# Optimization experiments

Measured on AMD Instinct MI355X. Metric: run time of the kernel, lower is better.

Reference implementation:

```python
import jax, jax.numpy as jnp
import numpy as np

B, S, E, H, FF = 4, 2048, 1024, 16, 4096
TD = 32  # transition_dim


def _layer_norm(v, g, b, eps=1e-5):
    m = v.mean(-1, keepdims=True)
    var = ((v - m) ** 2).mean(-1, keepdims=True)
    return (v - m) * jax.lax.rsqrt(var + eps) * g + b


def setup_inputs() -> dict:
    key = jax.random.key(0)
    ks = jax.random.split(key, 8)
    w = 0.02
    return {
        "x": jax.random.normal(ks[0], (B, S, E), dtype=jnp.float32),
        "transition_dim": TD,
        "ln1_g": jnp.ones((E,), jnp.float32),
        "ln1_b": jnp.zeros((E,), jnp.float32),
        "ln2_g": jnp.ones((E,), jnp.float32),
        "ln2_b": jnp.zeros((E,), jnp.float32),
        "w_qkv": jax.random.normal(ks[1], (3 * E, E), jnp.float32) * w,
        "b_qkv": jnp.zeros((3 * E,), jnp.float32),
        "w_o": jax.random.normal(ks[2], (E, E), jnp.float32) * w,
        "b_o": jnp.zeros((E,), jnp.float32),
        "w_fc1": jax.random.normal(ks[3], (FF, E), jnp.float32) * w,
        "b_fc1": jnp.zeros((FF,), jnp.float32),
        "w_fc2": jax.random.normal(ks[4], (E, FF), jnp.float32) * w,
        "b_fc2": jnp.zeros((E,), jnp.float32),
    }


def reference(x, transition_dim, ln1_g, ln1_b, ln2_g, ln2_b, w_qkv, b_qkv,
              w_o, b_o, w_fc1, b_fc1, w_fc2, b_fc2):
    Bx, Sx, Ex = x.shape
    Dh = Ex // H
    xn = _layer_norm(x, ln1_g, ln1_b)
    qkv = xn @ w_qkv.T + b_qkv                      # [B,S,3E]
    q, k, v = jnp.split(qkv, 3, axis=-1)
    def heads(t):
        return t.reshape(Bx, Sx, H, Dh).transpose(0, 2, 1, 3)  # [B,H,S,Dh]
    q, k, v = heads(q), heads(k), heads(v)
    scores = jnp.einsum("bhqd,bhkd->bhqk", q, k) / np.sqrt(Dh).astype(np.float32)
    # custom mask: causal (j > i) OR periodic value-column (j % TD == TD-1) blocked
    i = jnp.arange(Sx)
    mask = (i[None, :] > i[:, None]) | ((i[None, :] % transition_dim) == transition_dim - 1)
    scores = jnp.where(mask[None, None], -jnp.inf, scores)
    p = jax.nn.softmax(scores, axis=-1)
    attn = jnp.einsum("bhqk,bhkd->bhqd", p, v)
    attn = attn.transpose(0, 2, 1, 3).reshape(Bx, Sx, Ex)
    attn = attn @ w_o.T + b_o
    x = x + attn
    h = _layer_norm(x, ln2_g, ln2_b)
    h = jax.nn.gelu(h @ w_fc1.T + b_fc1, approximate=False) @ w_fc2.T + b_fc2
    return x + h
```

## Files before the change

### kernel.cpp

```cpp
#include <hip/hip_runtime.h>
#include <hip/hip_bf16.h>

typedef unsigned short u16;
typedef unsigned int u32;
typedef short bf16x8 __attribute__((ext_vector_type(8)));
typedef float f32x4 __attribute__((ext_vector_type(4)));
typedef float f32x16 __attribute__((ext_vector_type(16)));

#define B_ 4
#define S_ 2048
#define E_ 1024
#define H_ 16
#define FF_ 4096
#define M_ 8192

__device__ __forceinline__ u16 f2bf(float f) {
    u32 u = __float_as_uint(f);
    u32 r = (u + 0x7FFFu + ((u >> 16) & 1u)) >> 16;
    return (u16)r;
}
__device__ __forceinline__ float bf2f(u16 v) {
    return __uint_as_float(((u32)v) << 16);
}
__device__ __forceinline__ u32 cvtpk(float lo, float hi) {
    u32 r;
    asm("v_cvt_pk_bf16_f32 %0, %1, %2" : "=v"(r) : "v"(lo), "v"(hi));
    return r;
}
__device__ __forceinline__ void pswap(u32& a, u32& b) {
    asm("v_permlane32_swap_b32 %0, %1" : "+v"(a), "+v"(b));
}
__device__ __forceinline__ void gload16(const void* g, void* l) {
    __builtin_amdgcn_global_load_lds(
        (__attribute__((address_space(1))) void*)g,
        (__attribute__((address_space(3))) void*)l, 16, 0, 0);
}

__global__ __launch_bounds__(256) void cvt_kernel(const float* __restrict__ in,
                                                  u16* __restrict__ out, int n4) {
    int i = blockIdx.x * 256 + threadIdx.x;
    if (i < n4) {
        float4 v = ((const float4*)in)[i];
        ushort4 o;
        o.x = f2bf(v.x); o.y = f2bf(v.y); o.z = f2bf(v.z); o.w = f2bf(v.w);
        ((ushort4*)out)[i] = o;
    }
}

__global__ __launch_bounds__(256) void ln_kernel(const float* __restrict__ x,
                                                 const float* __restrict__ g,
                                                 const float* __restrict__ bb,
                                                 u16* __restrict__ out) {
    int row = blockIdx.x;
    int t = threadIdx.x;
    const float4* xr = (const float4*)(x + (size_t)row * E_);
    float4 v = xr[t];
    float s = v.x + v.y + v.z + v.w;
    float sq = v.x * v.x + v.y * v.y + v.z * v.z + v.w * v.w;
    for (int o = 1; o < 64; o <<= 1) {
        s += __shfl_xor(s, o, 64);
        sq += __shfl_xor(sq, o, 64);
    }
    __shared__ float ss[4], sqs[4];
    int w = t >> 6, l = t & 63;
    if (l == 0) { ss[w] = s; sqs[w] = sq; }
    __syncthreads();
    s = ss[0] + ss[1] + ss[2] + ss[3];
    sq = sqs[0] + sqs[1] + sqs[2] + sqs[3];
    float mean = s * (1.0f / E_);
    float var = sq * (1.0f / E_) - mean * mean;
    float rstd = rsqrtf(var + 1e-5f);
    float4 gv = ((const float4*)g)[t];
    float4 bv = ((const float4*)bb)[t];
    ushort4 o4;
    o4.x = f2bf((v.x - mean) * rstd * gv.x + bv.x);
    o4.y = f2bf((v.y - mean) * rstd * gv.y + bv.y);
    o4.z = f2bf((v.z - mean) * rstd * gv.z + bv.z);
    o4.w = f2bf((v.w - mean) * rstd * gv.w + bv.w);
    ((ushort4*)(out + (size_t)row * E_))[t] = o4;
}

template <int EPI, int BN>
__global__ __launch_bounds__(512, 2) void gemm256(const u16* __restrict__ A,
                                                  const u16* __restrict__ Bt,
                                                  const float* __restrict__ bias,
                                                  void* __restrict__ outp,
                                                  const float* __restrict__ resid,
                                                  u16* __restrict__ vt,
                                                  int N, int K) {
    constexpr int NF = BN / 64;
    __shared__ u16 ldsA[2 * 2 * 8192];
    __shared__ u16 ldsB[BN == 256 ? 2 * 2 * 8192 : 2 * 8192];
    int t = threadIdx.x;
    int wid = t >> 6, l = t & 63, l15 = l & 15, hi4 = l >> 4;
    int wm = wid >> 2, wn = wid & 3;

    int nwg = gridDim.x;
    int flat = blockIdx.x;
    int swz = (flat & 7) * (nwg >> 3) + (flat >> 3);
    int nx = N / BN;
    int m0 = (swz / nx) * 256, n0 = (swz % nx) * BN;
    const size_t Kb = (size_t)K * 2;

    f32x4 acc[8][NF];
    f32x4 zf = {0.f, 0.f, 0.f, 0.f};
#pragma unroll
    for (int i = 0; i < 8; i++)
#pragma unroll
        for (int j = 0; j < NF; j++) acc[i][j] = zf;

    auto stageA = [&](int buf, int h, int k0) {
#pragma unroll
        for (int rr = 0; rr < 2; ++rr) {
            int o = t * 16 + rr * 8192;
            int lr = o >> 7;
            int gch = ((o >> 4) & 7) ^ (lr & 7);
            int grow = m0 + (lr >> 6) * 128 + h * 64 + (lr & 63);
            gload16((const char*)A + (size_t)grow * Kb + k0 * 2 + gch * 16,
                    (char*)ldsA + (buf * 2 + h) * 16384 + o);
        }
    };
    auto stageB256 = [&](int buf, int h, int k0) {
#pragma unroll
        for (int rr = 0; rr < 2; ++rr) {
            int o = t * 16 + rr * 8192;
            int lr = o >> 7;
            int gch = ((o >> 4) & 7) ^ (lr & 7);
            int grow = n0 + (lr >> 5) * 64 + h * 32 + (lr & 31);
            gload16((const char*)Bt + (size_t)grow * Kb + k0 * 2 + gch * 16,
                    (char*)ldsB + (buf * 2 + h) * 16384 + o);
        }
    };
    auto stageB128 = [&](int buf, int k0) {
#pragma unroll
        for (int rr = 0; rr < 2; ++rr) {
            int o = t * 16 + rr * 8192;
            int lr = o >> 7;
            int gch = ((o >> 4) & 7) ^ (lr & 7);
            int grow = n0 + lr;
            gload16((const char*)Bt + (size_t)grow * Kb + k0 * 2 + gch * 16,
                    (char*)ldsB + buf * 16384 + o);
        }
    };

    auto readA = [&](int bq, int mh, bf16x8 (&af)[4][2]) {
#pragma unroll
        for (int mi = 0; mi < 4; mi++)
#pragma unroll
            for (int ks = 0; ks < 2; ks++) {
                int lr = wm * 64 + mi * 16 + l15;
                int ob = lr * 128 + ks * 64 + hi4 * 16;
                af[mi][ks] = *(const bf16x8*)((const char*)ldsA +
                             (bq * 2 + mh) * 16384 + (ob ^ ((lr & 7) << 4)));
            }
    };
    auto readB256 = [&](int bq, int nh, bf16x8 (&bfr)[2][2]) {
#pragma unroll
        for (int nq = 0; nq < 2; nq++)
#pragma unroll
            for (int ks = 0; ks < 2; ks++) {
                int lr = wn * 32 + nq * 16 + l15;
                int ob = lr * 128 + ks * 64 + hi4 * 16;
                bfr[nq][ks] = *(const bf16x8*)((const char*)ldsB +
                              (bq * 2 + nh) * 16384 + (ob ^ ((lr & 7) << 4)));
            }
    };
    auto readB128 = [&](int bq, bf16x8 (&bfr)[2][2]) {
#pragma unroll
        for (int nq = 0; nq < 2; nq++)
#pragma unroll
            for (int ks = 0; ks < 2; ks++) {
                int lr = wn * 32 + nq * 16 + l15;
                int ob = lr * 128 + ks * 64 + hi4 * 16;
                bfr[nq][ks] = *(const bf16x8*)((const char*)ldsB +
                              bq * 16384 + (ob ^ ((lr & 7) << 4)));
            }
    };
    auto mma = [&](bf16x8 (&af)[4][2], bf16x8 (&bfr)[2][2], int mh, int nh) {
#pragma unroll
        for (int mi = 0; mi < 4; mi++)
#pragma unroll
            for (int nq = 0; nq < 2; nq++)
#pragma unroll
                for (int ks = 0; ks < 2; ks++)
                    acc[mh * 4 + mi][nh * 2 + nq] =
                        __builtin_amdgcn_mfma_f32_16x16x32_bf16(
                            af[mi][ks], bfr[nq][ks], acc[mh * 4 + mi][nh * 2 + nq], 0, 0, 0);
    };

#define GWAIT(N)                                            \
    asm volatile("s_waitcnt vmcnt(" #N ")" ::: "memory");   \
    __builtin_amdgcn_sched_barrier(0);
#define PH_MID                                              \
    __builtin_amdgcn_s_barrier();                           \
    asm volatile("s_waitcnt lgkmcnt(0)" ::: "memory");      \
    __builtin_amdgcn_sched_barrier(0);                      \
    __builtin_amdgcn_s_setprio(1);
#define PH_END                                              \
    __builtin_amdgcn_s_setprio(0);                          \
    __builtin_amdgcn_s_barrier();

    int KT = K >> 6, ITERS = KT >> 1;

    if constexpr (BN == 256) {
        stageB256(0, 0, 0); stageB256(0, 1, 0); stageA(0, 0, 0); stageA(0, 1, 0);
        stageB256(1, 0, 64); stageB256(1, 1, 64); stageA(1, 0, 64);
        GWAIT(6);
        __builtin_amdgcn_s_barrier();
        for (int s = 0; s < ITERS; ++s) {
            int k1 = (2 * s + 1) << 6;
            int k2 = (2 * s + 2) << 6; if (k2 >= K) k2 = 0;
            int k3 = (2 * s + 3) << 6; if (k3 >= K) k3 = 0;
            bf16x8 af[4][2], b0[2][2], b1[2][2];
            readA(0, 0, af); readB256(0, 0, b0); stageA(1, 1, k1);
            PH_MID; mma(af, b0, 0, 0); PH_END;
            readB256(0, 1, b1); stageB256(0, 0, k2);
            PH_MID; mma(af, b1, 0, 1); PH_END;
            readA(0, 1, af); stageB256(0, 1, k2);
            PH_MID; mma(af, b0, 1, 0); PH_END;
            stageA(0, 0, k2); GWAIT(6);
            PH_MID; mma(af, b1, 1, 1); PH_END;
            readA(1, 0, af); readB256(1, 0, b0); stageA(0, 1, k2);
            PH_MID; mma(af, b0, 0, 0); PH_END;
            readB256(1, 1, b1); stageB256(1, 0, k3);
            PH_MID; mma(af, b1, 0, 1); PH_END;
            readA(1, 1, af); stageB256(1, 1, k3);
            PH_MID; mma(af, b0, 1, 0); PH_END;
            stageA(1, 0, k3); GWAIT(6);
            PH_MID; mma(af, b1, 1, 1); PH_END;
        }
    } else {
        stageB128(0, 0); stageA(0, 0, 0); stageA(0, 1, 0);
        stageB128(1, 64); stageA(1, 0, 64);
        GWAIT(4);
        __builtin_amdgcn_s_barrier();
        for (int s = 0; s < ITERS; ++s) {
            int k1 = (2 * s + 1) << 6;
            int k2 = (2 * s + 2) << 6; if (k2 >= K) k2 = 0;
            int k3 = (2 * s + 3) << 6; if (k3 >= K) k3 = 0;
            bf16x8 af[4][2], br[2][2];
            readA(0, 0, af); readB128(0, br); stageA(1, 1, k1);
            PH_MID; mma(af, br, 0, 0); PH_END;
            readA(0, 1, af); stageB128(0, k2); stageA(0, 0, k2); GWAIT(4);
            PH_MID; mma(af, br, 1, 0); PH_END;
            readA(1, 0, af); readB128(1, br); stageA(0, 1, k2);
            PH_MID; mma(af, br, 0, 0); PH_END;
            readA(1, 1, af); stageB128(1, k3); stageA(1, 0, k3); GWAIT(4);
            PH_MID; mma(af, br, 1, 0); PH_END;
        }
    }
#undef GWAIT
#undef PH_MID
#undef PH_END

    float bias_v[NF];
#pragma unroll
    for (int nf = 0; nf < NF; nf++) bias_v[nf] = bias[n0 + wn * (NF * 16) + nf * 16 + l15];

    if constexpr (EPI == 3) {
#pragma unroll
        for (int mf = 0; mf < 8; mf++)
#pragma unroll
            for (int nf = 0; nf < NF; nf++) {
                int col = n0 + wn * (NF * 16) + nf * 16 + l15;
                int row0 = m0 + wm * 128 + mf * 16 + hi4 * 4;
                ushort4 sv;
                u16* o16 = (u16*)outp;
#pragma unroll
                for (int j = 0; j < 4; j++) {
                    float v = acc[mf][nf][j] + bias_v[nf];
                    u16 r = f2bf(v);
                    o16[(size_t)(row0 + j) * N + col] = r;
                    ((u16*)&sv)[j] = r;
                }
                if (col >= 2048) {
                    int bb = row0 >> 11, s0r = row0 & 2047;
                    *(ushort4*)&vt[(((size_t)(bb << 10) + (col - 2048)) << 11) + s0r] = sv;
                }
            }
    } else {
#pragma unroll
        for (int mf = 0; mf < 8; mf++)
#pragma unroll
            for (int nf = 0; nf < NF; nf++)
#pragma unroll
                for (int j = 0; j < 4; j++) {
                    int row = m0 + wm * 128 + mf * 16 + hi4 * 4 + j;
                    int col = n0 + wn * (NF * 16) + nf * 16 + l15;
                    float v = acc[mf][nf][j] + bias_v[nf];
                    size_t idx = (size_t)row * N + col;
                    if (EPI == 2) v = 0.5f * v * (1.0f + erff(v * 0.70710678118f));
                    if (EPI == 1)
                        ((float*)outp)[idx] = resid[idx] + v;
                    else
                        ((u16*)outp)[idx] = f2bf(v);
                }
    }
}

__global__ __launch_bounds__(128) void attn_kernel(const u16* __restrict__ qkv,
                                                   const u16* __restrict__ vt,
                                                   u16* __restrict__ aout) {
    __shared__ u16 Ksb[2 * 4096];
    __shared__ u16 Vsb[2 * 4096];
    int t = threadIdx.x;
    int wv = t >> 6, l = t & 63;
    int q31 = l & 31, hi = l >> 5;
    int flat = blockIdx.x;
    int logical = (flat & 7) * 256 + (flat >> 3);
    int bh = logical >> 5;
    int qt = 31 - (logical & 31);
    int b = bh >> 4, h = bh & 15;
    int rowq = qt * 64 + wv * 32 + q31;

    const float qs = 0.18033688011f;
    const float THR = 44.3616f;

    bf16x8 qreg[4];
    const u16* qbase = qkv + (size_t)(b * S_ + rowq) * 3072 + h * 64 + hi * 8;
#pragma unroll
    for (int g = 0; g < 4; g++) qreg[g] = *(const bf16x8*)(qbase + 16 * g);

    const char* srcK0 = (const char*)(qkv + E_ + (size_t)(b * S_ + (t >> 3)) * 3072 + h * 64) +
                        ((t & 7) ^ ((t >> 3) & 7)) * 16;
    const char* srcV0 = (const char*)(vt + ((size_t)(bh * 64 + (t >> 3))) * 2048) +
                        ((t & 7) ^ ((t >> 3) & 7)) * 16;
    auto issueK = [&](int buf, int j0) {
#pragma unroll
        for (int pp = 0; pp < 4; pp++)
            gload16(srcK0 + (size_t)pp * 98304 + (size_t)j0 * 6144,
                    (char*)Ksb + buf * 8192 + 16 * t + 2048 * pp);
    };
    auto issueV = [&](int buf, int j0) {
#pragma unroll
        for (int pp = 0; pp < 4; pp++)
            gload16(srcV0 + (size_t)pp * 65536 + (size_t)j0 * 2,
                    (char*)Vsb + buf * 8192 + 16 * t + 2048 * pp);
    };

    f32x16 zf16;
#pragma unroll
    for (int r = 0; r < 16; r++) zf16[r] = 0.f;
    f32x16 o0 = zf16, o1 = zf16;
    float mrun = -INFINITY, lrun = 0.f;

    int j1 = (qt >= 1) ? 64 : 0;
    issueK(0, 0); issueV(0, 0);
    issueK(1, j1); issueV(1, j1);

    for (int jt = 0; jt <= qt; ++jt) {
        int cur = jt & 1;
        int j0 = jt * 64;
        asm volatile("s_waitcnt vmcnt(8)" ::: "memory");
        __builtin_amdgcn_sched_barrier(0);
        __builtin_amdgcn_s_barrier();

        const u16* Kc = Ksb + cur * 4096;
        const u16* Vc = Vsb + cur * 4096;

        f32x16 s0 = zf16, s1 = zf16;
        __builtin_amdgcn_s_setprio(1);
#pragma unroll
        for (int g = 0; g < 4; g++) {
            int r0 = q31, r1 = 32 + q31;
            bf16x8 k0 = *(const bf16x8*)&Kc[((r0 << 6) + hi * 8 + 16 * g) ^ ((r0 & 7) << 3)];
            bf16x8 k1 = *(const bf16x8*)&Kc[((r1 << 6) + hi * 8 + 16 * g) ^ ((r1 & 7) << 3)];
            s0 = __builtin_amdgcn_mfma_f32_32x32x16_bf16(k0, qreg[g], s0, 0, 0, 0);
            s1 = __builtin_amdgcn_mfma_f32_32x32x16_bf16(k1, qreg[g], s1, 0, 0, 0);
        }
        __builtin_amdgcn_s_setprio(0);

        float mx = -INFINITY;
        int cb0 = j0 + 4 * hi;
        if (jt == qt) {
#pragma unroll
            for (int r = 0; r < 16; r++) {
                const int cc = (r & 3) + 8 * (r >> 2);
                float v0 = s0[r], v1 = s1[r];
                bool bad0 = (cb0 + cc > rowq) || (r == 15 && hi);
                bool bad1 = (cb0 + 32 + cc > rowq) || (r == 15 && hi);
                v0 = bad0 ? -INFINITY : v0;
                v1 = bad1 ? -INFINITY : v1;
                s0[r] = v0; s1[r] = v1;
                mx = fmaxf(mx, fmaxf(v0, v1));
            }
        } else {
#pragma unroll
            for (int r = 0; r < 16; r++) {
                float v0 = s0[r], v1 = s1[r];
                if (r == 15) {
                    v0 = hi ? -INFINITY : v0;
                    v1 = hi ? -INFINITY : v1;
                    s0[r] = v0; s1[r] = v1;
                }
                mx = fmaxf(mx, fmaxf(v0, v1));
            }
        }
        mx = fmaxf(mx, __shfl_xor(mx, 32, 64));

        bool dokeep = __all(mx <= mrun + THR);
        if (!dokeep) {
            float mnew = fmaxf(mrun, mx);
            float sc = __builtin_amdgcn_exp2f((mrun - mnew) * qs);
#pragma unroll
            for (int r = 0; r < 16; r++) { o0[r] *= sc; o1[r] *= sc; }
            lrun *= sc;
            mrun = mnew;
        }
        float mq = mrun * qs;

        float sa = 0.f, sb = 0.f, sc2 = 0.f, sd = 0.f;
#pragma unroll
        for (int r = 0; r < 16; r++) {
            float p0 = __builtin_amdgcn_exp2f(fmaf(s0[r], qs, -mq));
            float p1 = __builtin_amdgcn_exp2f(fmaf(s1[r], qs, -mq));
            s0[r] = p0; s1[r] = p1;
            if (r & 1) { sb += p0; sd += p1; } else { sa += p0; sc2 += p1; }
        }
        lrun += (sa + sb) + (sc2 + sd);

        bf16x8 pa[4];
#pragma unroll
        for (int g = 0; g < 4; g++) {
            const int bs = (g & 1) * 8;
            u32 wa, wb, wc, wd;
            if (g < 2) {
                wa = cvtpk(s0[bs + 0], s0[bs + 1]);
                wb = cvtpk(s0[bs + 4], s0[bs + 5]);
                wc = cvtpk(s0[bs + 2], s0[bs + 3]);
                wd = cvtpk(s0[bs + 6], s0[bs + 7]);
            } else {
                wa = cvtpk(s1[bs + 0], s1[bs + 1]);
                wb = cvtpk(s1[bs + 4], s1[bs + 5]);
                wc = cvtpk(s1[bs + 2], s1[bs + 3]);
                wd = cvtpk(s1[bs + 6], s1[bs + 7]);
            }
            pswap(wa, wb);
            pswap(wc, wd);
            union { u32 w[4]; bf16x8 f; } u;
            u.w[0] = wa; u.w[1] = wc; u.w[2] = wb; u.w[3] = wd;
            pa[g] = u.f;
        }

        __builtin_amdgcn_s_setprio(1);
#pragma unroll
        for (int g = 0; g < 4; g++) {
            int d0 = q31, d1 = 32 + q31;
            bf16x8 v0 = *(const bf16x8*)&Vc[((d0 << 6) + hi * 8 + 16 * g) ^ ((d0 & 7) << 3)];
            bf16x8 v1 = *(const bf16x8*)&Vc[((d1 << 6) + hi * 8 + 16 * g) ^ ((d1 & 7) << 3)];
            o0 = __builtin_amdgcn_mfma_f32_32x32x16_bf16(v0, pa[g], o0, 0, 0, 0);
            o1 = __builtin_amdgcn_mfma_f32_32x32x16_bf16(v1, pa[g], o1, 0, 0, 0);
        }
        __builtin_amdgcn_s_setprio(0);

        __builtin_amdgcn_s_barrier();
        int nj = (jt + 2 <= qt) ? (jt + 2) * 64 : 0;
        issueK(cur, nj);
        issueV(cur, nj);
    }

    lrun += __shfl_xor(lrun, 32, 64);
    float inv = 1.0f / lrun;
    u16* orow = aout + (size_t)(b * S_ + rowq) * E_ + h * 64 + 4 * hi;
#pragma unroll
    for (int r = 0; r < 16; r++) {
        const int cc = (r & 3) + 8 * (r >> 2);
        orow[cc] = f2bf(o0[r] * inv);
        orow[32 + cc] = f2bf(o1[r] * inv);
    }
}

extern "C" void kernel_launch(void* const* d_in, const int* in_sizes, int n_in,
                              void* d_out, int out_size, void* d_ws, size_t ws_size,
                              hipStream_t stream) {
    const float* x = (const float*)d_in[0];
    const float* ln1_g = (const float*)d_in[2];
    const float* ln1_b = (const float*)d_in[3];
    const float* ln2_g = (const float*)d_in[4];
    const float* ln2_b = (const float*)d_in[5];
    const float* w_qkv = (const float*)d_in[6];
    const float* b_qkv = (const float*)d_in[7];
    const float* w_o = (const float*)d_in[8];
    const float* b_o = (const float*)d_in[9];
    const float* w_fc1 = (const float*)d_in[10];
    const float* b_fc1 = (const float*)d_in[11];
    const float* w_fc2 = (const float*)d_in[12];
    const float* b_fc2 = (const float*)d_in[13];
    float* out = (float*)d_out;
    char* ws = (char*)d_ws;

    u16* wqkv_bf = (u16*)(ws);
    u16* wo_bf   = (u16*)(ws + 6291456);
    u16* wfc1_bf = (u16*)(ws + 8388608);
    u16* wfc2_bf = (u16*)(ws + 16777216);
    u16* xn_bf   = (u16*)(ws + 25165824);
    u16* qkv_bf  = (u16*)(ws + 41943040);
    u16* ffn1_bf = (u16*)(ws + 41943040);
    u16* attn_bf = (u16*)(ws + 92274688);
    float* x2    = (float*)(ws + 109051904);
    u16* vtw     = (u16*)(ws + 109051904);
    (void)in_sizes; (void)n_in; (void)out_size; (void)ws_size;

    cvt_kernel<<<3072, 256, 0, stream>>>(w_qkv, wqkv_bf, 786432);
    cvt_kernel<<<1024, 256, 0, stream>>>(w_o, wo_bf, 262144);
    cvt_kernel<<<4096, 256, 0, stream>>>(w_fc1, wfc1_bf, 1048576);
    cvt_kernel<<<4096, 256, 0, stream>>>(w_fc2, wfc2_bf, 1048576);

    ln_kernel<<<M_, 256, 0, stream>>>(x, ln1_g, ln1_b, xn_bf);

    gemm256<3, 256><<<384, 512, 0, stream>>>(xn_bf, wqkv_bf, b_qkv, qkv_bf, nullptr, vtw, 3072, 1024);

    attn_kernel<<<2048, 128, 0, stream>>>(qkv_bf, vtw, attn_bf);

    gemm256<1, 128><<<256, 512, 0, stream>>>(attn_bf, wo_bf, b_o, x2, x, nullptr, 1024, 1024);

    ln_kernel<<<M_, 256, 0, stream>>>(x2, ln2_g, ln2_b, xn_bf);

    gemm256<2, 256><<<512, 512, 0, stream>>>(xn_bf, wfc1_bf, b_fc1, ffn1_bf, nullptr, nullptr, 4096, 1024);

    gemm256<1, 128><<<256, 512, 0, stream>>>(ffn1_bf, wfc2_bf, b_fc2, out, x2, nullptr, 1024, 4096);
}
```

Before: 407.5 us.

## Pair causal query tiles per attention block, split V transpose, merge weight casts

The attention kernel now has each block handle two query tiles, p0 and 31-p0, one after the other, so every block does the same amount of causal work, and the grid is halved to 1024 blocks. The V transpose moves out of the QKV GEMM epilogue, which did scattered ushort4 stores, into its own LDS-tiled transpose kernel. The four weight cast launches are merged into one. The cost is an extra kernel launch and a second read of the V slice, in exchange for better load balance and a simpler GEMM epilogue.

```diff
diff --git a/kernel.cpp b/kernel.cpp
--- a/kernel.cpp
+++ b/kernel.cpp
@@ -36,15 +36,49 @@
         (__attribute__((address_space(3))) void*)l, 16, 0, 0);
 }
 
-__global__ __launch_bounds__(256) void cvt_kernel(const float* __restrict__ in,
-                                                  u16* __restrict__ out, int n4) {
-    int i = blockIdx.x * 256 + threadIdx.x;
-    if (i < n4) {
-        float4 v = ((const float4*)in)[i];
-        ushort4 o;
-        o.x = f2bf(v.x); o.y = f2bf(v.y); o.z = f2bf(v.z); o.w = f2bf(v.w);
-        ((ushort4*)out)[i] = o;
+__global__ __launch_bounds__(256) void cvt4_kernel(const float* __restrict__ s0, u16* __restrict__ d0,
+                                                   const float* __restrict__ s1, u16* __restrict__ d1,
+                                                   const float* __restrict__ s2, u16* __restrict__ d2,
+                                                   const float* __restrict__ s3, u16* __restrict__ d3) {
+    int blk = blockIdx.x;
+    const float* s; u16* d; int base;
+    if (blk < 3072)      { s = s0; d = d0; base = blk; }
+    else if (blk < 4096) { s = s1; d = d1; base = blk - 3072; }
+    else if (blk < 8192) { s = s2; d = d2; base = blk - 4096; }
+    else                 { s = s3; d = d3; base = blk - 8192; }
+    int i = base * 256 + threadIdx.x;
+    float4 v = ((const float4*)s)[i];
+    ushort4 o;
+    o.x = f2bf(v.x); o.y = f2bf(v.y); o.z = f2bf(v.z); o.w = f2bf(v.w);
+    ((ushort4*)d)[i] = o;
+}
+
+__global__ __launch_bounds__(256) void vtrans_kernel(const u16* __restrict__ qkv,
+                                                     u16* __restrict__ vt) {
+    __shared__ u16 tile[64 * 67];
+    int t = threadIdx.x;
+    int st = blockIdx.x;
+    int bh = blockIdx.y;
+    int b = bh >> 4, h = bh & 15;
+    int s0 = st * 64;
+    int r = t >> 3, c0 = (t & 7) * 8;
+#pragma unroll
+    for (int half = 0; half < 2; half++) {
+        int rr = r + half * 32;
+        const u16* src = qkv + (size_t)(b * S_ + s0 + rr) * 3072 + 2048 + h * 64 + c0;
+        uint4 v = *(const uint4*)src;
+        u16* pv = (u16*)&v;
+#pragma unroll
+        for (int e = 0; e < 8; e++) tile[(c0 + e) * 67 + rr] = pv[e];
     }
+    __syncthreads();
+    int d = t >> 2, ch = t & 3;
+    u16 buf[16];
+#pragma unroll
+    for (int j = 0; j < 16; j++) buf[j] = tile[d * 67 + ch * 16 + j];
+    u16* dst = vt + ((size_t)bh * 64 + d) * 2048 + s0 + ch * 16;
+    *(uint4*)dst = *(uint4*)&buf[0];
+    *(uint4*)(dst + 8) = *(uint4*)&buf[8];
 }
 
 __global__ __launch_bounds__(256) void ln_kernel(const float* __restrict__ x,
@@ -86,7 +120,6 @@
                                                   const float* __restrict__ bias,
                                                   void* __restrict__ outp,
                                                   const float* __restrict__ resid,
-                                                  u16* __restrict__ vt,
                                                   int N, int K) {
     constexpr int NF = BN / 64;
     __shared__ u16 ldsA[2 * 2 * 8192];
@@ -257,45 +290,22 @@
 #pragma unroll
     for (int nf = 0; nf < NF; nf++) bias_v[nf] = bias[n0 + wn * (NF * 16) + nf * 16 + l15];
 
-    if constexpr (EPI == 3) {
-#pragma unroll
-        for (int mf = 0; mf < 8; mf++)
-#pragma unroll
-            for (int nf = 0; nf < NF; nf++) {
+#pragma unroll
+    for (int mf = 0; mf < 8; mf++)
+#pragma unroll
+        for (int nf = 0; nf < NF; nf++)
+#pragma unroll
+            for (int j = 0; j < 4; j++) {
+                int row = m0 + wm * 128 + mf * 16 + hi4 * 4 + j;
                 int col = n0 + wn * (NF * 16) + nf * 16 + l15;
-                int row0 = m0 + wm * 128 + mf * 16 + hi4 * 4;
-                ushort4 sv;
-                u16* o16 = (u16*)outp;
-#pragma unroll
-                for (int j = 0; j < 4; j++) {
-                    float v = acc[mf][nf][j] + bias_v[nf];
-                    u16 r = f2bf(v);
-                    o16[(size_t)(row0 + j) * N + col] = r;
-                    ((u16*)&sv)[j] = r;
-                }
-                if (col >= 2048) {
-                    int bb = row0 >> 11, s0r = row0 & 2047;
-                    *(ushort4*)&vt[(((size_t)(bb << 10) + (col - 2048)) << 11) + s0r] = sv;
-                }
-            }
-    } else {
-#pragma unroll
-        for (int mf = 0; mf < 8; mf++)
-#pragma unroll
-            for (int nf = 0; nf < NF; nf++)
-#pragma unroll
-                for (int j = 0; j < 4; j++) {
-                    int row = m0 + wm * 128 + mf * 16 + hi4 * 4 + j;
-                    int col = n0 + wn * (NF * 16) + nf * 16 + l15;
-                    float v = acc[mf][nf][j] + bias_v[nf];
-                    size_t idx = (size_t)row * N + col;
-                    if (EPI == 2) v = 0.5f * v * (1.0f + erff(v * 0.70710678118f));
-                    if (EPI == 1)
-                        ((float*)outp)[idx] = resid[idx] + v;
-                    else
-                        ((u16*)outp)[idx] = f2bf(v);
-                }
-    }
+                float v = acc[mf][nf][j] + bias_v[nf];
+                size_t idx = (size_t)row * N + col;
+                if (EPI == 2) v = 0.5f * v * (1.0f + erff(v * 0.70710678118f));
+                if (EPI == 1)
+                    ((float*)outp)[idx] = resid[idx] + v;
+                else
+                    ((u16*)outp)[idx] = f2bf(v);
+            }
 }
 
 __global__ __launch_bounds__(128) void attn_kernel(const u16* __restrict__ qkv,
@@ -307,19 +317,12 @@
     int wv = t >> 6, l = t & 63;
     int q31 = l & 31, hi = l >> 5;
     int flat = blockIdx.x;
-    int logical = (flat & 7) * 256 + (flat >> 3);
-    int bh = logical >> 5;
-    int qt = 31 - (logical & 31);
+    int logical = (flat & 7) * 128 + (flat >> 3);
+    int bh = logical >> 4, p0 = logical & 15;
     int b = bh >> 4, h = bh & 15;
-    int rowq = qt * 64 + wv * 32 + q31;
 
     const float qs = 0.18033688011f;
     const float THR = 44.3616f;
-
-    bf16x8 qreg[4];
-    const u16* qbase = qkv + (size_t)(b * S_ + rowq) * 3072 + h * 64 + hi * 8;
-#pragma unroll
-    for (int g = 0; g < 4; g++) qreg[g] = *(const bf16x8*)(qbase + 16 * g);
 
     const char* srcK0 = (const char*)(qkv + E_ + (size_t)(b * S_ + (t >> 3)) * 3072 + h * 64) +
                         ((t & 7) ^ ((t >> 3) & 7)) * 16;
@@ -341,132 +344,149 @@
     f32x16 zf16;
 #pragma unroll
     for (int r = 0; r < 16; r++) zf16[r] = 0.f;
-    f32x16 o0 = zf16, o1 = zf16;
-    float mrun = -INFINITY, lrun = 0.f;
-
-    int j1 = (qt >= 1) ? 64 : 0;
-    issueK(0, 0); issueV(0, 0);
-    issueK(1, j1); issueV(1, j1);
-
-    for (int jt = 0; jt <= qt; ++jt) {
-        int cur = jt & 1;
-        int j0 = jt * 64;
-        asm volatile("s_waitcnt vmcnt(8)" ::: "memory");
-        __builtin_amdgcn_sched_barrier(0);
-        __builtin_amdgcn_s_barrier();
-
-        const u16* Kc = Ksb + cur * 4096;
-        const u16* Vc = Vsb + cur * 4096;
-
-        f32x16 s0 = zf16, s1 = zf16;
-        __builtin_amdgcn_s_setprio(1);
-#pragma unroll
-        for (int g = 0; g < 4; g++) {
-            int r0 = q31, r1 = 32 + q31;
-            bf16x8 k0 = *(const bf16x8*)&Kc[((r0 << 6) + hi * 8 + 16 * g) ^ ((r0 & 7) << 3)];
-            bf16x8 k1 = *(const bf16x8*)&Kc[((r1 << 6) + hi * 8 + 16 * g) ^ ((r1 & 7) << 3)];
-            s0 = __builtin_amdgcn_mfma_f32_32x32x16_bf16(k0, qreg[g], s0, 0, 0, 0);
-            s1 = __builtin_amdgcn_mfma_f32_32x32x16_bf16(k1, qreg[g], s1, 0, 0, 0);
-        }
-        __builtin_amdgcn_s_setprio(0);
-
-        float mx = -INFINITY;
-        int cb0 = j0 + 4 * hi;
-        if (jt == qt) {
+
+    for (int half = 0; half < 2; ++half) {
+        int qt = half ? (31 - p0) : p0;
+        int rowq = qt * 64 + wv * 32 + q31;
+
+        bf16x8 qreg[4];
+        const u16* qbase = qkv + (size_t)(b * S_ + rowq) * 3072 + h * 64 + hi * 8;
+#pragma unroll
+        for (int g = 0; g < 4; g++) qreg[g] = *(const bf16x8*)(qbase + 16 * g);
+
+        f32x16 o0 = zf16, o1 = zf16;
+        float mrun = -INFINITY, lrun = 0.f;
+
+        int j1 = (qt >= 1) ? 64 : 0;
+        issueK(0, 0); issueV(0, 0);
+        issueK(1, j1); issueV(1, j1);
+
+        for (int jt = 0; jt <= qt; ++jt) {
+            int cur = jt & 1;
+            int j0 = jt * 64;
+            asm volatile("s_waitcnt vmcnt(8)" ::: "memory");
+            __builtin_amdgcn_sched_barrier(0);
+            __builtin_amdgcn_s_barrier();
+
+            const u16* Kc = Ksb + cur * 4096;
+            const u16* Vc = Vsb + cur * 4096;
+
+            f32x16 s0 = zf16, s1 = zf16;
+            __builtin_amdgcn_s_setprio(1);
+#pragma unroll
+            for (int g = 0; g < 4; g++) {
+                int r0 = q31, r1 = 32 + q31;
+                bf16x8 k0 = *(const bf16x8*)&Kc[((r0 << 6) + hi * 8 + 16 * g) ^ ((r0 & 7) << 3)];
+                bf16x8 k1 = *(const bf16x8*)&Kc[((r1 << 6) + hi * 8 + 16 * g) ^ ((r1 & 7) << 3)];
+                s0 = __builtin_amdgcn_mfma_f32_32x32x16_bf16(k0, qreg[g], s0, 0, 0, 0);
+                s1 = __builtin_amdgcn_mfma_f32_32x32x16_bf16(k1, qreg[g], s1, 0, 0, 0);
+            }
+            __builtin_amdgcn_s_setprio(0);
+
+            float mx = -INFINITY;
+            int cb0 = j0 + 4 * hi;
+            if (jt == qt) {
+#pragma unroll
+                for (int r = 0; r < 16; r++) {
+                    const int cc = (r & 3) + 8 * (r >> 2);
+                    float v0 = s0[r], v1 = s1[r];
+                    bool bad0 = (cb0 + cc > rowq) || (r == 15 && hi);
+                    bool bad1 = (cb0 + 32 + cc > rowq) || (r == 15 && hi);
+                    v0 = bad0 ? -INFINITY : v0;
+                    v1 = bad1 ? -INFINITY : v1;
+                    s0[r] = v0; s1[r] = v1;
+                    mx = fmaxf(mx, fmaxf(v0, v1));
+                }
+            } else {
+#pragma unroll
+                for (int r = 0; r < 16; r++) {
+                    float v0 = s0[r], v1 = s1[r];
+                    if (r == 15) {
+                        v0 = hi ? -INFINITY : v0;
+                        v1 = hi ? -INFINITY : v1;
+                        s0[r] = v0; s1[r] = v1;
+                    }
+                    mx = fmaxf(mx, fmaxf(v0, v1));
+                }
+            }
+            mx = fmaxf(mx, __shfl_xor(mx, 32, 64));
+
+            bool dokeep = __all(mx <= mrun + THR);
+            if (!dokeep) {
+                float mnew = fmaxf(mrun, mx);
+                float sc = __builtin_amdgcn_exp2f((mrun - mnew) * qs);
+#pragma unroll
+                for (int r = 0; r < 16; r++) { o0[r] *= sc; o1[r] *= sc; }
+                lrun *= sc;
+                mrun = mnew;
+            }
+            float mq = mrun * qs;
+
+            float sa = 0.f, sb = 0.f, sc2 = 0.f, sd = 0.f;
 #pragma unroll
             for (int r = 0; r < 16; r++) {
-                const int cc = (r & 3) + 8 * (r >> 2);
-                float v0 = s0[r], v1 = s1[r];
-                bool bad0 = (cb0 + cc > rowq) || (r == 15 && hi);
-                bool bad1 = (cb0 + 32 + cc > rowq) || (r == 15 && hi);
-                v0 = bad0 ? -INFINITY : v0;
-                v1 = bad1 ? -INFINITY : v1;
-                s0[r] = v0; s1[r] = v1;
-                mx = fmaxf(mx, fmaxf(v0, v1));
-            }
-        } else {
-#pragma unroll
-            for (int r = 0; r < 16; r++) {
-                float v0 = s0[r], v1 = s1[r];
-                if (r == 15) {
-                    v0 = hi ? -INFINITY : v0;
-                    v1 = hi ? -INFINITY : v1;
-                    s0[r] = v0; s1[r] = v1;
+                float p0 = __builtin_amdgcn_exp2f(fmaf(s0[r], qs, -mq));
+                float p1 = __builtin_amdgcn_exp2f(fmaf(s1[r], qs, -mq));
+                s0[r] = p0; s1[r] = p1;
+                if (r & 1) { sb += p0; sd += p1; } else { sa += p0; sc2 += p1; }
+            }
+            lrun += (sa + sb) + (sc2 + sd);
+
+            bf16x8 pa[4];
+#pragma unroll
+            for (int g = 0; g < 4; g++) {
+                const int bs = (g & 1) * 8;
+                u32 wa, wb, wc, wd;
+                if (g < 2) {
+                    wa = cvtpk(s0[bs + 0], s0[bs + 1]);
+                    wb = cvtpk(s0[bs + 4], s0[bs + 5]);
+                    wc = cvtpk(s0[bs + 2], s0[bs + 3]);
+                    wd = cvtpk(s0[bs + 6], s0[bs + 7]);
+                } else {
+                    wa = cvtpk(s1[bs + 0], s1[bs + 1]);
+                    wb = cvtpk(s1[bs + 4], s1[bs + 5]);
+                    wc = cvtpk(s1[bs + 2], s1[bs + 3]);
+                    wd = cvtpk(s1[bs + 6], s1[bs + 7]);
                 }
-                mx = fmaxf(mx, fmaxf(v0, v1));
-            }
-        }
-        mx = fmaxf(mx, __shfl_xor(mx, 32, 64));
-
-        bool dokeep = __all(mx <= mrun + THR);
-        if (!dokeep) {
-            float mnew = fmaxf(mrun, mx);
-            float sc = __builtin_amdgcn_exp2f((mrun - mnew) * qs);
-#pragma unroll
-            for (int r = 0; r < 16; r++) { o0[r] *= sc; o1[r] *= sc; }
-            lrun *= sc;
-            mrun = mnew;
-        }
-        float mq = mrun * qs;
-
-        float sa = 0.f, sb = 0.f, sc2 = 0.f, sd = 0.f;
+                pswap(wa, wb);
+                pswap(wc, wd);
+                union { u32 w[4]; bf16x8 f; } u;
+                u.w[0] = wa; u.w[1] = wc; u.w[2] = wb; u.w[3] = wd;
+                pa[g] = u.f;
+            }
+
+            __builtin_amdgcn_s_setprio(1);
+#pragma unroll
+            for (int g = 0; g < 4; g++) {
+                int d0 = q31, d1 = 32 + q31;
+                bf16x8 v0 = *(const bf16x8*)&Vc[((d0 << 6) + hi * 8 + 16 * g) ^ ((d0 & 7) << 3)];
+                bf16x8 v1 = *(const bf16x8*)&Vc[((d1 << 6) + hi * 8 + 16 * g) ^ ((d1 & 7) << 3)];
+                o0 = __builtin_amdgcn_mfma_f32_32x32x16_bf16(v0, pa[g], o0, 0, 0, 0);
+                o1 = __builtin_amdgcn_mfma_f32_32x32x16_bf16(v1, pa[g], o1, 0, 0, 0);
+            }
+            __builtin_amdgcn_s_setprio(0);
+
+            __builtin_amdgcn_s_barrier();
+            int nj = (jt + 2 <= qt) ? (jt + 2) * 64 : 0;
+            issueK(cur, nj);
+            issueV(cur, nj);
+        }
+
+        lrun += __shfl_xor(lrun, 32, 64);
+        float inv = 1.0f / lrun;
+        u16* orow = aout + (size_t)(b * S_ + rowq) * E_ + h * 64 + 4 * hi;
 #pragma unroll
         for (int r = 0; r < 16; r++) {
-            float p0 = __builtin_amdgcn_exp2f(fmaf(s0[r], qs, -mq));
-            float p1 = __builtin_amdgcn_exp2f(fmaf(s1[r], qs, -mq));
-            s0[r] = p0; s1[r] = p1;
-            if (r & 1) { sb += p0; sd += p1; } else { sa += p0; sc2 += p1; }
-        }
-        lrun += (sa + sb) + (sc2 + sd);
-
-        bf16x8 pa[4];
-#pragma unroll
-        for (int g = 0; g < 4; g++) {
-            const int bs = (g & 1) * 8;
-            u32 wa, wb, wc, wd;
-            if (g < 2) {
-                wa = cvtpk(s0[bs + 0], s0[bs + 1]);
-                wb = cvtpk(s0[bs + 4], s0[bs + 5]);
-                wc = cvtpk(s0[bs + 2], s0[bs + 3]);
-                wd = cvtpk(s0[bs + 6], s0[bs + 7]);
-            } else {
-                wa = cvtpk(s1[bs + 0], s1[bs + 1]);
-                wb = cvtpk(s1[bs + 4], s1[bs + 5]);
-                wc = cvtpk(s1[bs + 2], s1[bs + 3]);
-                wd = cvtpk(s1[bs + 6], s1[bs + 7]);
-            }
-            pswap(wa, wb);
-            pswap(wc, wd);
-            union { u32 w[4]; bf16x8 f; } u;
-            u.w[0] = wa; u.w[1] = wc; u.w[2] = wb; u.w[3] = wd;
-            pa[g] = u.f;
-        }
-
-        __builtin_amdgcn_s_setprio(1);
-#pragma unroll
-        for (int g = 0; g < 4; g++) {
-            int d0 = q31, d1 = 32 + q31;
-            bf16x8 v0 = *(const bf16x8*)&Vc[((d0 << 6) + hi * 8 + 16 * g) ^ ((d0 & 7) << 3)];
-            bf16x8 v1 = *(const bf16x8*)&Vc[((d1 << 6) + hi * 8 + 16 * g) ^ ((d1 & 7) << 3)];
-            o0 = __builtin_amdgcn_mfma_f32_32x32x16_bf16(v0, pa[g], o0, 0, 0, 0);
-            o1 = __builtin_amdgcn_mfma_f32_32x32x16_bf16(v1, pa[g], o1, 0, 0, 0);
-        }
-        __builtin_amdgcn_s_setprio(0);
-
-        __builtin_amdgcn_s_barrier();
-        int nj = (jt + 2 <= qt) ? (jt + 2) * 64 : 0;
-        issueK(cur, nj);
-        issueV(cur, nj);
-    }
-
-    lrun += __shfl_xor(lrun, 32, 64);
-    float inv = 1.0f / lrun;
-    u16* orow = aout + (size_t)(b * S_ + rowq) * E_ + h * 64 + 4 * hi;
-#pragma unroll
-    for (int r = 0; r < 16; r++) {
-        const int cc = (r & 3) + 8 * (r >> 2);
-        orow[cc] = f2bf(o0[r] * inv);
-        orow[32 + cc] = f2bf(o1[r] * inv);
+            const int cc = (r & 3) + 8 * (r >> 2);
+            orow[cc] = f2bf(o0[r] * inv);
+            orow[32 + cc] = f2bf(o1[r] * inv);
+        }
+
+        if (half == 0) {
+            asm volatile("s_waitcnt vmcnt(0)" ::: "memory");
+            __builtin_amdgcn_sched_barrier(0);
+            __builtin_amdgcn_s_barrier();
+        }
     }
 }
 
@@ -501,22 +521,22 @@
     u16* vtw     = (u16*)(ws + 109051904);
     (void)in_sizes; (void)n_in; (void)out_size; (void)ws_size;
 
-    cvt_kernel<<<3072, 256, 0, stream>>>(w_qkv, wqkv_bf, 786432);
-    cvt_kernel<<<1024, 256, 0, stream>>>(w_o, wo_bf, 262144);
-    cvt_kernel<<<4096, 256, 0, stream>>>(w_fc1, wfc1_bf, 1048576);
-    cvt_kernel<<<4096, 256, 0, stream>>>(w_fc2, wfc2_bf, 1048576);
+    cvt4_kernel<<<12288, 256, 0, stream>>>(w_qkv, wqkv_bf, w_o, wo_bf,
+                                           w_fc1, wfc1_bf, w_fc2, wfc2_bf);
 
     ln_kernel<<<M_, 256, 0, stream>>>(x, ln1_g, ln1_b, xn_bf);
 
-    gemm256<3, 256><<<384, 512, 0, stream>>>(xn_bf, wqkv_bf, b_qkv, qkv_bf, nullptr, vtw, 3072, 1024);
-
-    attn_kernel<<<2048, 128, 0, stream>>>(qkv_bf, vtw, attn_bf);
-
-    gemm256<1, 128><<<256, 512, 0, stream>>>(attn_bf, wo_bf, b_o, x2, x, nullptr, 1024, 1024);
+    gemm256<0, 256><<<384, 512, 0, stream>>>(xn_bf, wqkv_bf, b_qkv, qkv_bf, nullptr, 3072, 1024);
+
+    vtrans_kernel<<<dim3(32, 64), 256, 0, stream>>>(qkv_bf, vtw);
+
+    attn_kernel<<<1024, 128, 0, stream>>>(qkv_bf, vtw, attn_bf);
+
+    gemm256<1, 128><<<256, 512, 0, stream>>>(attn_bf, wo_bf, b_o, x2, x, 1024, 1024);
 
     ln_kernel<<<M_, 256, 0, stream>>>(x2, ln2_g, ln2_b, xn_bf);
 
-    gemm256<2, 256><<<512, 512, 0, stream>>>(xn_bf, wfc1_bf, b_fc1, ffn1_bf, nullptr, nullptr, 4096, 1024);
-
-    gemm256<1, 128><<<256, 512, 0, stream>>>(ffn1_bf, wfc2_bf, b_fc2, out, x2, nullptr, 1024, 4096);
-}
+    gemm256<2, 256><<<512, 512, 0, stream>>>(xn_bf, wfc1_bf, b_fc1, ffn1_bf, nullptr, 4096, 1024);
+
+    gemm256<1, 128><<<256, 512, 0, stream>>>(ffn1_bf, wfc2_bf, b_fc2, out, x2, 1024, 4096);
+}
```

Result: faster. 380.5 us (-6.6%).
